# Kernel optimization log

Hardware: AMD Instinct MI355X
Metric: run time of the kernel (lower is better)

The kernel has to match this reference:

```python
import jax, jax.numpy as jnp
import numpy as np

NUM_ELMT = 64
INPUT_DIM = 16
BOUND = 50.0
MESH_RATIO = 1.2
N_POINTS = 1_048_576


def _build_mesh():
    m = NUM_ELMT
    one_step = BOUND * (MESH_RATIO - 1.0) / (MESH_RATIO ** (m / 2) - 1.0)
    idx = np.arange(-m / 2, m / 2 + 1)
    mesh = (MESH_RATIO ** np.abs(idx) - 1.0) / (MESH_RATIO - 1.0) * one_step * np.sign(idx)
    mesh_norm = (mesh + BOUND) / (2.0 * BOUND)
    mesh_norm = np.concatenate([[0.0], mesh_norm[1:-1], [1.0]]).astype(np.float32)
    elmt_size = (mesh_norm[1:] - mesh_norm[:-1]).astype(np.float32)
    return jnp.asarray(mesh_norm), jnp.asarray(elmt_size)


def setup_inputs() -> dict:
    key = jax.random.key(0)
    k1, k2 = jax.random.split(key)
    x = jax.random.uniform(k1, (N_POINTS, INPUT_DIM), jnp.float32, minval=-BOUND, maxval=BOUND)
    pdj = jnp.ones((N_POINTS, 1), jnp.float32)
    sldj = jnp.zeros((N_POINTS, 1), jnp.float32)
    log_p = 0.1 * jax.random.normal(k2, (NUM_ELMT - 1, INPUT_DIM), jnp.float32)
    mesh_norm, elmt_size = _build_mesh()
    return {"x": x, "pdj": pdj, "sldj": sldj, "log_p": log_p,
            "mesh_norm": mesh_norm, "elmt_size": elmt_size}


def _normalize_pdf(log_p, elmt_size):
    # elmt_size: (M,) -> (M,1) column, log_p: (M-1, D)
    es = elmt_size[:, None]
    ep = jnp.exp(log_p)
    px = ep * (es[:-1] + es[1:]) / 2.0
    px = ep * (1.0 - es[0]) / jnp.sum(px, axis=0, keepdims=True)
    p0 = jnp.ones((1, log_p.shape[1]), log_p.dtype)
    pdf_norm = jnp.concatenate([p0, px, p0], axis=0)            # (M+1, D)
    cell = (pdf_norm[:-1] + pdf_norm[1:]) / 2.0 * es            # (M, D)
    # F_ref[i] = sum(cell[:i]); single cumsum instead of the O(M^2) torch loop
    F_ref = jnp.concatenate([jnp.zeros_like(p0), jnp.cumsum(cell, axis=0)[:-1]], axis=0)  # (M, D)
    return pdf_norm, F_ref


def reference(x, pdj, sldj, log_p, mesh_norm, elmt_size):
    pdf_norm, F_ref = _normalize_pdf(log_p, elmt_size)
    xn = (x + BOUND) / (2.0 * BOUND)                            # (N, D) in [0,1]
    k = jnp.searchsorted(mesh_norm, xn, side='left')            # (N, D), torch right=False
    cover = (k != 0) & (k != NUM_ELMT + 1)
    k = jnp.clip(k, 1, NUM_ELMT)
    km1 = k - 1
    v1 = jnp.take_along_axis(pdf_norm, km1, axis=0)             # pdf at lower node
    v2 = jnp.take_along_axis(pdf_norm, k, axis=0)               # pdf at upper node
    xmodi = xn - mesh_norm[km1]                                 # offset inside element
    h = elmt_size[km1]                                          # element width
    F_pre = jnp.take_along_axis(F_ref, km1, axis=0)             # CDF at lower node
    y = jnp.where(cover, F_pre + xmodi * xmodi * 0.5 * (v2 - v1) / h + xmodi * v1, xn)
    abs_det = jnp.where(cover, xmodi * (v2 - v1) / h + v1, 1.0)
    pdj_out = pdj * jnp.prod(abs_det, axis=-1, keepdims=True)
    sldj_out = sldj + jnp.sum(jnp.log(abs_det), axis=-1, keepdims=True)
    x_out = y * 2.0 * BOUND - BOUND
    return (x_out, pdj_out, sldj_out)
```

## Files before the change

### kernel.cpp

```cpp
#include <hip/hip_runtime.h>
#include <math.h>
#include <stdint.h>


namespace {
constexpr int DIM = 16;
constexpr int ME  = 64;
constexpr float BOUNDF = 50.0f;
constexpr float K1      = 6.8164378f;
constexpr float INV_L2R = 3.8017840f;
constexpr int NBIN = 66;
constexpr int ROWF = 68;
constexpr int COEF_FLOATS = NBIN * ROWF;
constexpr int EP_BASE = COEF_FLOATS - 63 * DIM;
}

__global__ __launch_bounds__(256) void nll_kernel(
    const float* __restrict__ x,
    const float* __restrict__ pdj,
    const float* __restrict__ sldj,
    const float* __restrict__ log_p,
    const float* __restrict__ mesh_norm,
    float* __restrict__ out,
    int npts, int npairs)
{
  __shared__ __align__(16) float co[COEF_FLOATS];
  __shared__ float s_mesh[ME + 1];

  const int tid = threadIdx.x;

  if (tid <= ME) s_mesh[tid] = mesh_norm[tid];
  for (int i = tid; i < 63 * DIM; i += 256)
    co[EP_BASE + i] = __expf(log_p[i]);
  __syncthreads();

  const int wv = tid >> 6, lane = tid & 63;
  float epv[4];
#pragma unroll
  for (int i = 0; i < 4; ++i)
    epv[i] = (lane < 63) ? co[EP_BASE + lane * DIM + (4 * wv + i)] : 0.f;
  const float mj  = s_mesh[lane];
  const float mj1 = s_mesh[lane + 1];
  const float mj2 = s_mesh[(lane + 2 > ME) ? ME : (lane + 2)];
  const float es0 = s_mesh[1] - s_mesh[0];
  __syncthreads();

  const float h = mj1 - mj;
#pragma unroll
  for (int i = 0; i < 4; ++i) {
    const int d = 4 * wv + i;
    const float ep = epv[i];
    float ss = (lane < 63) ? ep * (mj2 - mj) : 0.f;
    ss += __shfl_xor(ss, 1);  ss += __shfl_xor(ss, 2);  ss += __shfl_xor(ss, 4);
    ss += __shfl_xor(ss, 8);  ss += __shfl_xor(ss, 16); ss += __shfl_xor(ss, 32);
    const float scale = (1.0f - es0) / (0.5f * ss);
    const float cur = (lane < 63) ? ep * scale : 1.0f;
    float prev = __shfl_up(cur, 1);
    if (lane == 0) prev = 1.0f;
    const float cell = (prev + cur) * 0.5f * h;
    float v = cell, o;
    o = __shfl_up(v, 1);  if (lane >= 1)  v += o;
    o = __shfl_up(v, 2);  if (lane >= 2)  v += o;
    o = __shfl_up(v, 4);  if (lane >= 4)  v += o;
    o = __shfl_up(v, 8);  if (lane >= 8)  v += o;
    o = __shfl_up(v, 16); if (lane >= 16) v += o;
    o = __shfl_up(v, 32); if (lane >= 32) v += o;
    const float F = v - cell;
    const float A = 0.5f * (cur - prev) / h;
    const float B = fmaf(-(A + A), mj, prev);
    const float D = fmaf(mj, fmaf(mj, A, -prev), F);
    *reinterpret_cast<float4*>(&co[(lane + 1) * ROWF + 4 * d]) = make_float4(A, B, D, A + A);
  }
  if (tid < 32) {
    const int row = (tid >> 4) ? (NBIN - 1) : 0;
    const int d = tid & 15;
    *reinterpret_cast<float4*>(&co[row * ROWF + 4 * d]) = make_float4(0.f, 1.f, 0.f, 0.f);
  }
  __syncthreads();

  const int tpg = gridDim.x * blockDim.x;
  const float4* __restrict__ x4 = reinterpret_cast<const float4*>(x);
  float4* __restrict__ out4 = reinterpret_cast<float4*>(out);
  const int np16 = npts * DIM;

  int t = blockIdx.x * blockDim.x + tid;
  if (t >= npairs) return;

  float4 a0 = x4[2 * t], a1 = x4[2 * t + 1];
  float aps = (t & 1) ? sldj[t >> 1] : pdj[t >> 1];
  int tB = t + tpg;
  bool hasB = tB < npairs;
  float4 b0, b1; float bps = 0.f;
  if (hasB) {
    b0 = x4[2 * tB]; b1 = x4[2 * tB + 1];
    bps = (tB & 1) ? sldj[tB >> 1] : pdj[tB >> 1];
  }

  while (true) {
    const int tC = t + 2 * tpg;
    const bool hasC = tC < npairs;
    float4 c0, c1; float cps = 0.f;
    if (hasC) {
      c0 = x4[2 * tC]; c1 = x4[2 * tC + 1];
      cps = (tC & 1) ? sldj[tC >> 1] : pdj[tC >> 1];
    }

    const int p  = t >> 1;
    const int hh = t & 1;
    const int dbase = hh << 5;
    const float vals[8] = {a0.x, a0.y, a0.z, a0.w, a1.x, a1.y, a1.z, a1.w};

    float xn[8];
    int   idx[8];
#pragma unroll
    for (int j = 0; j < 8; ++j) {
      const float val = vals[j];
      xn[j] = fmaf(val, 0.01f, 0.5f);
      const float u = fmaf(fabsf(val), K1, 1.0f);
      const float n = __log2f(u) * INV_L2R;
      int k = 32 + (int)ceilf(copysignf(n, val));
      k = k < 0 ? 0 : (k > NBIN - 1 ? NBIN - 1 : k);
      idx[j] = k * ROWF + dbase + (j << 2);
    }

    float4 cf[8];
#pragma unroll
    for (int j = 0; j < 8; ++j)
      cf[j] = *reinterpret_cast<const float4*>(&co[idx[j]]);

    float yv[8], dt[8];
#pragma unroll
    for (int j = 0; j < 8; ++j) {
      const float z = xn[j];
      yv[j] = fmaf(fmaf(z, fmaf(z, cf[j].x, cf[j].y), cf[j].z), 2.0f * BOUNDF, -BOUNDF);
      dt[j] = fmaf(z, cf[j].w, cf[j].y);
    }
    const float prod = ((dt[0] * dt[1]) * (dt[2] * dt[3])) *
                       ((dt[4] * dt[5]) * (dt[6] * dt[7]));

    out4[2 * t]     = make_float4(yv[0], yv[1], yv[2], yv[3]);
    out4[2 * t + 1] = make_float4(yv[4], yv[5], yv[6], yv[7]);

    const float full = prod * __shfl_xor(prod, 1);
    const float res  = hh ? (aps + __logf(full)) : (aps * full);
    out[np16 + hh * npts + p] = res;

    if (!hasB) break;
    t = tB; a0 = b0; a1 = b1; aps = bps;
    tB = tC; hasB = hasC; b0 = c0; b1 = c1; bps = cps;
  }
}

extern "C" void kernel_launch(void* const* d_in, const int* in_sizes, int n_in,
                              void* d_out, int out_size, void* d_ws, size_t ws_size,
                              hipStream_t stream) {
  const float* x    = (const float*)d_in[0];
  const float* pdj  = (const float*)d_in[1];
  const float* sldj = (const float*)d_in[2];
  const float* lp   = (const float*)d_in[3];
  const float* mesh = (const float*)d_in[4];
  float* out = (float*)d_out;

  const int npts   = in_sizes[0] / DIM;
  const int npairs = npts * 2;
  const int block  = 256;
  int grid = 2048;
  const int needed = (npairs + block - 1) / block;
  if (needed < grid) grid = needed;

  hipLaunchKernelGGL(nll_kernel, dim3(grid), dim3(block), 0, stream,
                     x, pdj, sldj, lp, mesh, out, npts, npairs);
}
```

Measured before the change: 32.85 us.

## Split table build into setup kernel and use one-pair-per-thread main kernel

Coefficient table construction moves out of every block into a single-block setup kernel that writes the table to workspace. The main kernel copies the finished table into shared memory and handles exactly one point-pair per thread over a full grid, dropping the grid-stride loop and its software prefetch. This removes redundant per-block exp/scan work but adds a second launch with a serial dependency, and there are now many more blocks each doing a table load.

```diff
diff --git a/kernel.cpp b/kernel.cpp
--- a/kernel.cpp
+++ b/kernel.cpp
@@ -11,45 +11,30 @@
 constexpr float INV_L2R = 3.8017840f;
 constexpr int NBIN = 66;
 constexpr int ROWF = 68;
-constexpr int COEF_FLOATS = NBIN * ROWF;
-constexpr int EP_BASE = COEF_FLOATS - 63 * DIM;
+constexpr int TABLE_FLOATS = NBIN * ROWF;
 }
 
-__global__ __launch_bounds__(256) void nll_kernel(
-    const float* __restrict__ x,
-    const float* __restrict__ pdj,
-    const float* __restrict__ sldj,
+__global__ __launch_bounds__(256) void nll_setup(
     const float* __restrict__ log_p,
     const float* __restrict__ mesh_norm,
-    float* __restrict__ out,
-    int npts, int npairs)
+    float* __restrict__ table)
 {
-  __shared__ __align__(16) float co[COEF_FLOATS];
   __shared__ float s_mesh[ME + 1];
-
   const int tid = threadIdx.x;
-
   if (tid <= ME) s_mesh[tid] = mesh_norm[tid];
-  for (int i = tid; i < 63 * DIM; i += 256)
-    co[EP_BASE + i] = __expf(log_p[i]);
   __syncthreads();
 
   const int wv = tid >> 6, lane = tid & 63;
-  float epv[4];
-#pragma unroll
-  for (int i = 0; i < 4; ++i)
-    epv[i] = (lane < 63) ? co[EP_BASE + lane * DIM + (4 * wv + i)] : 0.f;
   const float mj  = s_mesh[lane];
   const float mj1 = s_mesh[lane + 1];
   const float mj2 = s_mesh[(lane + 2 > ME) ? ME : (lane + 2)];
   const float es0 = s_mesh[1] - s_mesh[0];
-  __syncthreads();
+  const float h = mj1 - mj;
 
-  const float h = mj1 - mj;
 #pragma unroll
   for (int i = 0; i < 4; ++i) {
     const int d = 4 * wv + i;
-    const float ep = epv[i];
+    const float ep = (lane < 63) ? __expf(log_p[lane * DIM + d]) : 0.f;
     float ss = (lane < 63) ? ep * (mj2 - mj) : 0.f;
     ss += __shfl_xor(ss, 1);  ss += __shfl_xor(ss, 2);  ss += __shfl_xor(ss, 4);
     ss += __shfl_xor(ss, 8);  ss += __shfl_xor(ss, 16); ss += __shfl_xor(ss, 32);
@@ -69,86 +54,88 @@
     const float A = 0.5f * (cur - prev) / h;
     const float B = fmaf(-(A + A), mj, prev);
     const float D = fmaf(mj, fmaf(mj, A, -prev), F);
-    *reinterpret_cast<float4*>(&co[(lane + 1) * ROWF + 4 * d]) = make_float4(A, B, D, A + A);
+    *reinterpret_cast<float4*>(&table[(lane + 1) * ROWF + 4 * d]) =
+        make_float4(A, B, D, A + A);
   }
   if (tid < 32) {
     const int row = (tid >> 4) ? (NBIN - 1) : 0;
     const int d = tid & 15;
-    *reinterpret_cast<float4*>(&co[row * ROWF + 4 * d]) = make_float4(0.f, 1.f, 0.f, 0.f);
+    *reinterpret_cast<float4*>(&table[row * ROWF + 4 * d]) =
+        make_float4(0.f, 1.f, 0.f, 0.f);
+  }
+}
+
+__global__ __launch_bounds__(256) void nll_main(
+    const float* __restrict__ x,
+    const float* __restrict__ pdj,
+    const float* __restrict__ sldj,
+    const float* __restrict__ table,
+    float* __restrict__ out,
+    int npts, int npairs)
+{
+  __shared__ __align__(16) float co[TABLE_FLOATS];
+
+  const int tid = threadIdx.x;
+  {
+    const float4* t4 = reinterpret_cast<const float4*>(table);
+    float4* c4 = reinterpret_cast<float4*>(co);
+#pragma unroll
+    for (int i = 0; i < 5; ++i) {
+      const int idx = tid + 256 * i;
+      if (idx < TABLE_FLOATS / 4) c4[idx] = t4[idx];
+    }
   }
   __syncthreads();
 
-  const int tpg = gridDim.x * blockDim.x;
+  const int t = blockIdx.x * blockDim.x + tid;
+  if (t >= npairs) return;
+
   const float4* __restrict__ x4 = reinterpret_cast<const float4*>(x);
   float4* __restrict__ out4 = reinterpret_cast<float4*>(out);
   const int np16 = npts * DIM;
 
-  int t = blockIdx.x * blockDim.x + tid;
-  if (t >= npairs) return;
+  const int p  = t >> 1;
+  const int hh = t & 1;
+  const int dbase = hh << 5;
+  const float4 xa = x4[2 * t];
+  const float4 xb = x4[2 * t + 1];
+  const float ps = hh ? sldj[p] : pdj[p];
+  const float vals[8] = {xa.x, xa.y, xa.z, xa.w, xb.x, xb.y, xb.z, xb.w};
 
-  float4 a0 = x4[2 * t], a1 = x4[2 * t + 1];
-  float aps = (t & 1) ? sldj[t >> 1] : pdj[t >> 1];
-  int tB = t + tpg;
-  bool hasB = tB < npairs;
-  float4 b0, b1; float bps = 0.f;
-  if (hasB) {
-    b0 = x4[2 * tB]; b1 = x4[2 * tB + 1];
-    bps = (tB & 1) ? sldj[tB >> 1] : pdj[tB >> 1];
+  float xn[8];
+  int   idx[8];
+#pragma unroll
+  for (int j = 0; j < 8; ++j) {
+    const float val = vals[j];
+    xn[j] = fmaf(val, 0.01f, 0.5f);
+    const float u = fmaf(fabsf(val), K1, 1.0f);
+    const float n = __log2f(u) * INV_L2R;
+    int k = 32 + (int)ceilf(copysignf(n, val));
+    k = k < 0 ? 0 : (k > NBIN - 1 ? NBIN - 1 : k);
+    idx[j] = k * ROWF + dbase + (j << 2);
   }
 
-  while (true) {
-    const int tC = t + 2 * tpg;
-    const bool hasC = tC < npairs;
-    float4 c0, c1; float cps = 0.f;
-    if (hasC) {
-      c0 = x4[2 * tC]; c1 = x4[2 * tC + 1];
-      cps = (tC & 1) ? sldj[tC >> 1] : pdj[tC >> 1];
-    }
+  float4 cf[8];
+#pragma unroll
+  for (int j = 0; j < 8; ++j)
+    cf[j] = *reinterpret_cast<const float4*>(&co[idx[j]]);
 
-    const int p  = t >> 1;
-    const int hh = t & 1;
-    const int dbase = hh << 5;
-    const float vals[8] = {a0.x, a0.y, a0.z, a0.w, a1.x, a1.y, a1.z, a1.w};
+  float yv[8], dt[8];
+#pragma unroll
+  for (int j = 0; j < 8; ++j) {
+    const float z = xn[j];
+    yv[j] = fmaf(fmaf(z, fmaf(z, cf[j].x, cf[j].y), cf[j].z), 2.0f * BOUNDF, -BOUNDF);
+    dt[j] = fmaf(z, cf[j].w, cf[j].y);
+  }
+  const float prod = ((dt[0] * dt[1]) * (dt[2] * dt[3])) *
+                     ((dt[4] * dt[5]) * (dt[6] * dt[7]));
 
-    float xn[8];
-    int   idx[8];
-#pragma unroll
-    for (int j = 0; j < 8; ++j) {
-      const float val = vals[j];
-      xn[j] = fmaf(val, 0.01f, 0.5f);
-      const float u = fmaf(fabsf(val), K1, 1.0f);
-      const float n = __log2f(u) * INV_L2R;
-      int k = 32 + (int)ceilf(copysignf(n, val));
-      k = k < 0 ? 0 : (k > NBIN - 1 ? NBIN - 1 : k);
-      idx[j] = k * ROWF + dbase + (j << 2);
-    }
+  out4[2 * t]     = make_float4(yv[0], yv[1], yv[2], yv[3]);
+  out4[2 * t + 1] = make_float4(yv[4], yv[5], yv[6], yv[7]);
 
-    float4 cf[8];
-#pragma unroll
-    for (int j = 0; j < 8; ++j)
-      cf[j] = *reinterpret_cast<const float4*>(&co[idx[j]]);
-
-    float yv[8], dt[8];
-#pragma unroll
-    for (int j = 0; j < 8; ++j) {
-      const float z = xn[j];
-      yv[j] = fmaf(fmaf(z, fmaf(z, cf[j].x, cf[j].y), cf[j].z), 2.0f * BOUNDF, -BOUNDF);
-      dt[j] = fmaf(z, cf[j].w, cf[j].y);
-    }
-    const float prod = ((dt[0] * dt[1]) * (dt[2] * dt[3])) *
-                       ((dt[4] * dt[5]) * (dt[6] * dt[7]));
-
-    out4[2 * t]     = make_float4(yv[0], yv[1], yv[2], yv[3]);
-    out4[2 * t + 1] = make_float4(yv[4], yv[5], yv[6], yv[7]);
-
-    const float full = prod * __shfl_xor(prod, 1);
-    const float res  = hh ? (aps + __logf(full)) : (aps * full);
-    out[np16 + hh * npts + p] = res;
-
-    if (!hasB) break;
-    t = tB; a0 = b0; a1 = b1; aps = bps;
-    tB = tC; hasB = hasC; b0 = c0; b1 = c1; bps = cps;
-  }
+  const float full = prod * __shfl_xor(prod, 1);
+  const float res  = hh ? (ps + __logf(full)) : (ps * full);
+  out[np16 + hh * npts + p] = res;
 }
 
 extern "C" void kernel_launch(void* const* d_in, const int* in_sizes, int n_in,
@@ -159,15 +146,15 @@
   const float* sldj = (const float*)d_in[2];
   const float* lp   = (const float*)d_in[3];
   const float* mesh = (const float*)d_in[4];
-  float* out = (float*)d_out;
+  float* out   = (float*)d_out;
+  float* table = (float*)d_ws;
 
   const int npts   = in_sizes[0] / DIM;
   const int npairs = npts * 2;
   const int block  = 256;
-  int grid = 2048;
-  const int needed = (npairs + block - 1) / block;
-  if (needed < grid) grid = needed;
+  const int grid   = (npairs + block - 1) / block;
 
-  hipLaunchKernelGGL(nll_kernel, dim3(grid), dim3(block), 0, stream,
-                     x, pdj, sldj, lp, mesh, out, npts, npairs);
+  hipLaunchKernelGGL(nll_setup, dim3(1), dim3(block), 0, stream, lp, mesh, table);
+  hipLaunchKernelGGL(nll_main, dim3(grid), dim3(block), 0, stream,
+                     x, pdj, sldj, table, out, npts, npairs);
 }
```

After: 35.85 us. 9.2% more time.
